# Kernel optimization log

Hardware: AMD Instinct MI355X
Metric: run time of the kernel (lower is better)

The kernel has to match this reference:

```python
import jax, jax.numpy as jnp
import numpy as np

EPS = 1e-9


def setup_inputs() -> dict:
    key = jax.random.key(0)
    k1, k2, k3 = jax.random.split(key, 3)
    B, N, E, F_IN, F_OUT = 8, 2048, 1024, 256, 256
    x = jax.random.normal(k1, (B, N, F_IN), dtype=jnp.float32)
    H = jax.random.uniform(k2, (B, N, E), dtype=jnp.float32)  # soft incidence matrix
    weight = jax.random.normal(k3, (F_IN, F_OUT), dtype=jnp.float32) * (1.0 / np.sqrt(F_OUT))
    return {"x": x, "H": H, "weight": weight}


def reference(x, H, weight):
    # x: [B, N, Fin], H: [B, N, E], weight: [Fin, Fout]
    # Torch builds diag_embed(Dv_inv)/diag_embed(De_inv) and uses dense bmm;
    # mathematically identical to elementwise row-scaling, done here directly.
    Dv = jnp.sum(H, axis=2)                       # [B, N]  (= bmm(H, ones))
    De = jnp.sum(H, axis=1)                       # [B, E]
    Dv_inv = 1.0 / (Dv + EPS)
    De_inv = 1.0 / (De + EPS)
    xw = jnp.matmul(x, weight)                    # [B, N, Fout]
    HTX = jnp.einsum('bne,bnf->bef', H, xw)       # H^T @ X
    HDeHTX = jnp.einsum('bne,bef->bnf', H, De_inv[:, :, None] * HTX)
    out = Dv_inv[:, :, None] * HDeHTX             # [B, N, Fout]
    # dropout in eval mode (identity); relu kept
    return jax.nn.relu(out)
```

## Files before the change

### kernel.cpp

```cpp
#include <hip/hip_runtime.h>
#include <stdint.h>


typedef __bf16 bf16x8 __attribute__((ext_vector_type(8)));
typedef float f32x4 __attribute__((ext_vector_type(4)));

#define PADK 72

__device__ __forceinline__ uint16_t f2b(float f) {
  __bf16 h = (__bf16)f;
  return __builtin_bit_cast(uint16_t, h);
}

__device__ __forceinline__ f32x4 mfma16(bf16x8 a, bf16x8 b, f32x4 c) {
  return __builtin_amdgcn_mfma_f32_16x16x32_bf16(a, b, c, 0, 0, 0);
}

__device__ __forceinline__ void gload16(const void* src, void* dst) {
  __builtin_amdgcn_global_load_lds(
      (const __attribute__((address_space(1))) void*)src,
      (__attribute__((address_space(3))) void*)dst, 16, 0, 0);
}

#define PIPE_WAITN(N) do { \
    asm volatile("s_waitcnt vmcnt(" #N ")" ::: "memory"); \
    __builtin_amdgcn_s_barrier(); \
    __builtin_amdgcn_sched_barrier(0); \
  } while (0)

__global__ __launch_bounds__(256) void k_prep_w(const float* __restrict__ W,
    uint16_t* __restrict__ Wt) {
  __shared__ __align__(16) uint16_t T[64 * 68];
  const int k0 = blockIdx.x * 64, f0 = blockIdx.y * 64;
  const int t = threadIdx.x;
  const int r0 = (t >> 4) * 4, cc = (t & 15) * 4;
  float vv[4][4];
  #pragma unroll
  for (int i = 0; i < 4; ++i) {
    float4 q = *(const float4*)(W + (size_t)(k0 + r0 + i) * 256 + f0 + cc);
    vv[i][0] = q.x; vv[i][1] = q.y; vv[i][2] = q.z; vv[i][3] = q.w;
  }
  #pragma unroll
  for (int j = 0; j < 4; ++j) {
    union { uint16_t s[4]; uint2 u; } p;
    #pragma unroll
    for (int i = 0; i < 4; ++i) p.s[i] = f2b(vv[i][j]);
    *(uint2*)&T[(cc + j) * 68 + r0] = p.u;
  }
  __syncthreads();
  const int er = t >> 2, c2 = (t & 3) * 16;
  union { uint16_t s[16]; uint4 q[2]; } o;
  #pragma unroll
  for (int m = 0; m < 4; ++m)
    *(uint2*)&o.s[m * 4] = *(const uint2*)&T[er * 68 + c2 + m * 4];
  uint16_t* dst = Wt + (size_t)(f0 + er) * 256 + k0 + c2;
  *(uint4*)dst = o.q[0];
  *(uint4*)(dst + 8) = o.q[1];
}

__global__ __launch_bounds__(256) void k_prep_h(const float* __restrict__ H,
    uint16_t* __restrict__ Hbt, uint16_t* __restrict__ Hb,
    float* __restrict__ DvPart, float* __restrict__ DePart) {
  __shared__ __align__(16) uint16_t T[64 * 68];
  __shared__ float cs[4][64];
  const int n0 = blockIdx.x * 64, e0 = blockIdx.y * 64, b = blockIdx.z;
  const int t = threadIdx.x, lane = t & 63, wave = t >> 6;
  const int r0 = (t >> 4) * 4;
  const int cc = (t & 15) * 4;
  float vv[4][4];
  float dv[4];
  float de0 = 0.f, de1 = 0.f, de2 = 0.f, de3 = 0.f;
  #pragma unroll
  for (int i = 0; i < 4; ++i) {
    float4 q = *(const float4*)(H + ((size_t)b * 2048 + n0 + r0 + i) * 1024 + e0 + cc);
    vv[i][0] = q.x; vv[i][1] = q.y; vv[i][2] = q.z; vv[i][3] = q.w;
    float rs = (q.x + q.y) + (q.z + q.w);
    rs += __shfl_xor(rs, 1); rs += __shfl_xor(rs, 2);
    rs += __shfl_xor(rs, 4); rs += __shfl_xor(rs, 8);
    dv[i] = rs;
    de0 += q.x; de1 += q.y; de2 += q.z; de3 += q.w;
  }
  #pragma unroll
  for (int i = 0; i < 4; ++i) {
    union { uint16_t s[4]; uint2 u; } p;
    #pragma unroll
    for (int j = 0; j < 4; ++j) p.s[j] = f2b(vv[i][j]);
    *(uint2*)(Hb + ((size_t)b * 2048 + n0 + r0 + i) * 1024 + e0 + cc) = p.u;
  }
  #pragma unroll
  for (int j = 0; j < 4; ++j) {
    union { uint16_t s[4]; uint2 u; } p;
    #pragma unroll
    for (int i = 0; i < 4; ++i) p.s[i] = f2b(vv[i][j]);
    *(uint2*)&T[(cc + j) * 68 + r0] = p.u;
  }
  de0 += __shfl_xor(de0, 16); de0 += __shfl_xor(de0, 32);
  de1 += __shfl_xor(de1, 16); de1 += __shfl_xor(de1, 32);
  de2 += __shfl_xor(de2, 16); de2 += __shfl_xor(de2, 32);
  de3 += __shfl_xor(de3, 16); de3 += __shfl_xor(de3, 32);
  if (lane < 16) *(float4*)&cs[wave][cc] = make_float4(de0, de1, de2, de3);
  if ((lane & 15) == 0) {
    #pragma unroll
    for (int i = 0; i < 4; ++i)
      DvPart[((size_t)b * 2048 + n0 + r0 + i) * 16 + blockIdx.y] = dv[i];
  }
  __syncthreads();
  const int er = t >> 2, c2 = (t & 3) * 16;
  union { uint16_t s[16]; uint4 q[2]; } o;
  #pragma unroll
  for (int m = 0; m < 4; ++m)
    *(uint2*)&o.s[m * 4] = *(const uint2*)&T[er * 68 + c2 + m * 4];
  uint16_t* dst = Hbt + ((size_t)b * 1024 + e0 + er) * 2048 + n0 + c2;
  *(uint4*)dst = o.q[0];
  *(uint4*)(dst + 8) = o.q[1];
  if (t < 64) {
    float s = (cs[0][t] + cs[1][t]) + (cs[2][t] + cs[3][t]);
    DePart[((size_t)b * 1024 + e0 + t) * 32 + blockIdx.x] = s;
  }
}

__global__ __launch_bounds__(256) void k_gemm1(const float* __restrict__ X,
    const uint16_t* __restrict__ Wt, uint16_t* __restrict__ XWt) {
  __shared__ __align__(16) uint16_t As[2][128 * 64];
  __shared__ __align__(16) uint16_t Bs[2][64 * PADK];
  const int n0 = blockIdx.x * 64, f0 = blockIdx.y * 128, b = blockIdx.z;
  const int t = threadIdx.x, lane = t & 63, wave = t >> 6;
  const int l15 = lane & 15, lq = lane >> 4;
  const int rlane = lane >> 3;
  const int srcswz = ((lane & 7) ^ rlane) << 3;
  const uint16_t* Ag = Wt + (size_t)f0 * 256;
  const int br = t >> 2, kc = (t & 3) * 16;
  const float* Xg = X + ((size_t)b * 2048 + n0 + br) * 256 + kc;
  float4 RX[4];
  auto stageA = [&](uint16_t* Ad, int kt) {
    const int k0 = kt * 64;
    #pragma unroll
    for (int i = 0; i < 4; ++i) {
      const int r = wave * 32 + i * 8;
      gload16(Ag + (size_t)(r + rlane) * 256 + k0 + srcswz, Ad + r * 64);
    }
  };
  auto gloadB = [&](int kt) {
    const float* s = Xg + kt * 64;
    #pragma unroll
    for (int q = 0; q < 4; ++q) RX[q] = *(const float4*)(s + q * 4);
  };
  auto writeB = [&](uint16_t* Bd) {
    uint16_t* d = Bd + br * PADK + kc;
    const float* f = (const float*)RX;
    #pragma unroll
    for (int q = 0; q < 2; ++q) {
      union { uint16_t s[8]; uint4 u; } p;
      #pragma unroll
      for (int j = 0; j < 8; ++j) p.s[j] = f2b(f[q * 8 + j]);
      *(uint4*)(d + q * 8) = p.u;
    }
  };
  f32x4 acc[4][2] = {};
  auto compute = [&](const uint16_t* Ad, const uint16_t* Bd) {
    #pragma unroll
    for (int h = 0; h < 2; ++h) {
      bf16x8 af[4], bf[2];
      #pragma unroll
      for (int i = 0; i < 4; ++i) {
        const int r = (wave >> 1) * 64 + i * 16 + l15;
        af[i] = *(const bf16x8*)(Ad + r * 64 + ((((h << 2) | lq) ^ (r & 7)) << 3));
      }
      #pragma unroll
      for (int j = 0; j < 2; ++j) {
        const int r = (wave & 1) * 32 + j * 16 + l15;
        bf[j] = *(const bf16x8*)(Bd + r * PADK + h * 32 + lq * 8);
      }
      #pragma unroll
      for (int i = 0; i < 4; ++i)
        #pragma unroll
        for (int j = 0; j < 2; ++j)
          acc[i][j] = mfma16(af[i], bf[j], acc[i][j]);
    }
  };
  stageA(As[0], 0); gloadB(0); writeB(Bs[0]);
  __syncthreads();
  for (int kt = 0; kt < 4; kt += 2) {
    stageA(As[1], kt + 1); gloadB(kt + 1);
    compute(As[0], Bs[0]);
    writeB(Bs[1]);
    __syncthreads();
    if (kt + 2 < 4) { stageA(As[0], kt + 2); gloadB(kt + 2); }
    compute(As[1], Bs[1]);
    if (kt + 2 < 4) writeB(Bs[0]);
    __syncthreads();
  }
  #pragma unroll
  for (int i = 0; i < 4; ++i) {
    const int fr = f0 + (wave >> 1) * 64 + i * 16 + lq * 4;
    #pragma unroll
    for (int j = 0; j < 2; ++j) {
      const int col = n0 + (wave & 1) * 32 + j * 16 + l15;
      #pragma unroll
      for (int reg = 0; reg < 4; ++reg)
        XWt[((size_t)b * 256 + fr + reg) * 2048 + col] = f2b(acc[i][j][reg]);
    }
  }
}

__global__ __launch_bounds__(512) void k_gemm2(const uint16_t* __restrict__ Hbt,
    const uint16_t* __restrict__ XWt, const float* __restrict__ DePart,
    uint16_t* __restrict__ Yt) {
  __shared__ __align__(16) uint16_t As[3][256 * 32];
  __shared__ __align__(16) uint16_t Bs[3][64 * 32];
  __shared__ float sde[64];
  const int e0 = blockIdx.x * 64, b = blockIdx.z;
  const int t = threadIdx.x, lane = t & 63, wave = t >> 6;
  const int l15 = lane & 15, lq = lane >> 4;
  const int wf = wave >> 1, we = wave & 1;
  const int ri = lane >> 2, slot = lane & 3;
  const int ksw = (slot ^ ((ri >> 1) & 3)) * 8;
  const uint16_t* Ag = XWt + (size_t)b * 256 * 2048;
  const uint16_t* Bg = Hbt + ((size_t)b * 1024 + e0) * 2048;
  auto stage = [&](uint16_t* Ad, uint16_t* Bd, int kt) {
    const int k0 = kt * 32;
    const int a0 = wave * 2;
    gload16(Ag + (size_t)(a0 * 16 + ri) * 2048 + k0 + ksw, Ad + a0 * 512);
    gload16(Ag + (size_t)(a0 * 16 + 16 + ri) * 2048 + k0 + ksw, Ad + (a0 + 1) * 512);
    const int bb = wave >> 1;
    gload16(Bg + (size_t)(bb * 16 + ri) * 2048 + k0 + ksw, Bd + bb * 512);
  };
  f32x4 acc[4][2] = {};
  auto compute = [&](const uint16_t* Ad, const uint16_t* Bd) {
    bf16x8 af[4], bf[2];
    #pragma unroll
    for (int i = 0; i < 4; ++i) {
      const int r = wf * 64 + i * 16 + l15;
      af[i] = *(const bf16x8*)(Ad + r * 32 + ((lq ^ ((r >> 1) & 3)) * 8));
    }
    #pragma unroll
    for (int j = 0; j < 2; ++j) {
      const int r = we * 32 + j * 16 + l15;
      bf[j] = *(const bf16x8*)(Bd + r * 32 + ((lq ^ ((r >> 1) & 3)) * 8));
    }
    #pragma unroll
    for (int i = 0; i < 4; ++i)
      #pragma unroll
      for (int j = 0; j < 2; ++j)
        acc[i][j] = mfma16(af[i], bf[j], acc[i][j]);
  };
  if (t < 64) {
    const float* p = DePart + ((size_t)b * 1024 + e0 + t) * 32;
    float4 a0 = *(const float4*)(p + 0),  a1 = *(const float4*)(p + 4);
    float4 a2 = *(const float4*)(p + 8),  a3 = *(const float4*)(p + 12);
    float4 a4 = *(const float4*)(p + 16), a5 = *(const float4*)(p + 20);
    float4 a6 = *(const float4*)(p + 24), a7 = *(const float4*)(p + 28);
    float s = (((a0.x + a0.y) + (a0.z + a0.w)) + ((a1.x + a1.y) + (a1.z + a1.w)))
            + (((a2.x + a2.y) + (a2.z + a2.w)) + ((a3.x + a3.y) + (a3.z + a3.w)))
            + ((((a4.x + a4.y) + (a4.z + a4.w)) + ((a5.x + a5.y) + (a5.z + a5.w)))
            + (((a6.x + a6.y) + (a6.z + a6.w)) + ((a7.x + a7.y) + (a7.z + a7.w))));
    sde[t] = 1.f / (s + 1e-9f);
  }
  stage(As[0], Bs[0], 0);
  stage(As[1], Bs[1], 1);
  __syncthreads();
  const int NT = 64;
  uint16_t *cA = As[0], *nA = As[1], *fA = As[2];
  uint16_t *cB = Bs[0], *nB = Bs[1], *fB = Bs[2];
  for (int kt = 0; kt < NT - 2; ++kt) {
    stage(fA, fB, kt + 2);
    compute(cA, cB);
    PIPE_WAITN(3);
    uint16_t* t1 = cA; cA = nA; nA = fA; fA = t1;
    uint16_t* t2 = cB; cB = nB; nB = fB; fB = t2;
  }
  compute(cA, cB);
  PIPE_WAITN(0);
  compute(nA, nB);
  #pragma unroll
  for (int i = 0; i < 4; ++i) {
    const int fr = wf * 64 + i * 16 + lq * 4;
    #pragma unroll
    for (int j = 0; j < 2; ++j) {
      const int el = we * 32 + j * 16 + l15;
      const float sc = sde[el];
      uint16_t* dst = Yt + ((size_t)b * 256 + fr) * 1024 + e0 + el;
      #pragma unroll
      for (int reg = 0; reg < 4; ++reg)
        dst[(size_t)reg * 1024] = f2b(acc[i][j][reg] * sc);
    }
  }
}

__global__ __launch_bounds__(256) void k_gemm3(const uint16_t* __restrict__ Hb,
    const uint16_t* __restrict__ Yt, const float* __restrict__ DvPart,
    float* __restrict__ out) {
  __shared__ __align__(16) uint16_t As[3][128 * 32];
  __shared__ __align__(16) uint16_t Bs[3][128 * 32];
  __shared__ float sdv[128];
  const int n0 = blockIdx.x * 128, f0 = blockIdx.y * 128, b = blockIdx.z;
  const int t = threadIdx.x, lane = t & 63, wave = t >> 6;
  const int l15 = lane & 15, lq = lane >> 4;
  const int wn = wave >> 1, wf = wave & 1;
  const int ri = lane >> 2, slot = lane & 3;
  const int ksw = (slot ^ ((ri >> 1) & 3)) * 8;
  const uint16_t* Ag = Hb + ((size_t)b * 2048 + n0) * 1024;
  const uint16_t* Bg = Yt + ((size_t)b * 256 + f0) * 1024;
  auto stage = [&](uint16_t* Ad, uint16_t* Bd, int kt) {
    const int k0 = kt * 32;
    const int c0 = wave * 2;
    #pragma unroll
    for (int i = 0; i < 2; ++i) {
      gload16(Ag + (size_t)((c0 + i) * 16 + ri) * 1024 + k0 + ksw, Ad + (c0 + i) * 512);
      gload16(Bg + (size_t)((c0 + i) * 16 + ri) * 1024 + k0 + ksw, Bd + (c0 + i) * 512);
    }
  };
  f32x4 acc[4][4] = {};
  auto compute = [&](const uint16_t* Ad, const uint16_t* Bd) {
    bf16x8 af[4], bf[4];
    #pragma unroll
    for (int i = 0; i < 4; ++i) {
      const int r = wn * 64 + i * 16 + l15;
      af[i] = *(const bf16x8*)(Ad + r * 32 + ((lq ^ ((r >> 1) & 3)) * 8));
    }
    #pragma unroll
    for (int j = 0; j < 4; ++j) {
      const int r = wf * 64 + j * 16 + l15;
      bf[j] = *(const bf16x8*)(Bd + r * 32 + ((lq ^ ((r >> 1) & 3)) * 8));
    }
    #pragma unroll
    for (int i = 0; i < 4; ++i)
      #pragma unroll
      for (int j = 0; j < 4; ++j)
        acc[i][j] = mfma16(af[i], bf[j], acc[i][j]);
  };
  if (t < 128) {
    const float* p = DvPart + ((size_t)b * 2048 + n0 + t) * 16;
    float4 a0 = *(const float4*)(p + 0),  a1 = *(const float4*)(p + 4);
    float4 a2 = *(const float4*)(p + 8),  a3 = *(const float4*)(p + 12);
    float s = (((a0.x + a0.y) + (a0.z + a0.w)) + ((a1.x + a1.y) + (a1.z + a1.w)))
            + (((a2.x + a2.y) + (a2.z + a2.w)) + ((a3.x + a3.y) + (a3.z + a3.w)));
    sdv[t] = 1.f / (s + 1e-9f);
  }
  stage(As[0], Bs[0], 0);
  stage(As[1], Bs[1], 1);
  __syncthreads();
  const int NT = 32;
  uint16_t *cA = As[0], *nA = As[1], *fA = As[2];
  uint16_t *cB = Bs[0], *nB = Bs[1], *fB = Bs[2];
  for (int kt = 0; kt < NT - 2; ++kt) {
    stage(fA, fB, kt + 2);
    compute(cA, cB);
    PIPE_WAITN(4);
    uint16_t* t1 = cA; cA = nA; nA = fA; fA = t1;
    uint16_t* t2 = cB; cB = nB; nB = fB; fB = t2;
  }
  compute(cA, cB);
  PIPE_WAITN(0);
  compute(nA, nB);
  #pragma unroll
  for (int i = 0; i < 4; ++i) {
    const int nl = wn * 64 + i * 16 + lq * 4;
    #pragma unroll
    for (int reg = 0; reg < 4; ++reg) {
      const int row = n0 + nl + reg;
      const float sc = sdv[nl + reg];
      #pragma unroll
      for (int j = 0; j < 4; ++j) {
        const int col = f0 + wf * 64 + j * 16 + l15;
        const float v = acc[i][j][reg] * sc;
        out[((size_t)b * 2048 + row) * 256 + col] = v > 0.f ? v : 0.f;
      }
    }
  }
}

extern "C" void kernel_launch(void* const* d_in, const int* in_sizes, int n_in,
                              void* d_out, int out_size, void* d_ws, size_t ws_size,
                              hipStream_t stream) {
  (void)in_sizes; (void)n_in; (void)out_size;
  const float* x = (const float*)d_in[0];
  const float* H = (const float*)d_in[1];
  const float* W = (const float*)d_in[2];
  float* out = (float*)d_out;

  if (ws_size < 81920000) return;
  char* ws = (char*)d_ws;
  uint16_t* Hbt    = (uint16_t*)(ws);
  uint16_t* Hb     = (uint16_t*)(ws + 33554432);
  uint16_t* XWt    = (uint16_t*)(ws + 67108864);
  uint16_t* Yt     = (uint16_t*)(ws + 75497472);
  float*    DvPart = (float*)(ws + 79691776);
  float*    DePart = (float*)(ws + 80740352);
  uint16_t* Wt     = (uint16_t*)(ws + 81788928);

  k_prep_w<<<dim3(4, 4),      256, 0, stream>>>(W, Wt);
  k_prep_h<<<dim3(32, 16, 8), 256, 0, stream>>>(H, Hbt, Hb, DvPart, DePart);
  k_gemm1 <<<dim3(32, 2, 8),  256, 0, stream>>>(x, Wt, XWt);
  k_gemm2 <<<dim3(16, 1, 8),  512, 0, stream>>>(Hbt, XWt, DePart, Yt);
  k_gemm3 <<<dim3(16, 2, 8),  256, 0, stream>>>(Hb, Yt, DvPart, out);
}
```

Before: 92.38 us.

## Retile gemm2 into 64x128 tiles with K=64 steps and more blocks

The H^T·XW GEMM now uses 256-thread blocks, each computing a 64(F)×128(E) output tile, in place of 512-thread blocks that covered all 256 features for 64 edges. The K step doubles to 64, with an 8-way XOR swizzle in LDS and a deeper wait count. The grid grows from 128 to 256 blocks to fill more CUs and halve the barriers per K. In exchange, each block re-reads H tiles across 4 F-blocks, which raises global and L2 traffic for H.

```diff
diff --git a/kernel.cpp b/kernel.cpp
--- a/kernel.cpp
+++ b/kernel.cpp
@@ -203,48 +203,56 @@
   }
 }
 
-__global__ __launch_bounds__(512) void k_gemm2(const uint16_t* __restrict__ Hbt,
+__global__ __launch_bounds__(256) void k_gemm2(const uint16_t* __restrict__ Hbt,
     const uint16_t* __restrict__ XWt, const float* __restrict__ DePart,
     uint16_t* __restrict__ Yt) {
-  __shared__ __align__(16) uint16_t As[3][256 * 32];
-  __shared__ __align__(16) uint16_t Bs[3][64 * 32];
-  __shared__ float sde[64];
-  const int e0 = blockIdx.x * 64, b = blockIdx.z;
+  __shared__ __align__(16) uint16_t As[3][64 * 64];
+  __shared__ __align__(16) uint16_t Bs[3][128 * 64];
+  __shared__ float sde[128];
+  const int e0 = blockIdx.x * 128, f0 = blockIdx.y * 64, b = blockIdx.z;
   const int t = threadIdx.x, lane = t & 63, wave = t >> 6;
   const int l15 = lane & 15, lq = lane >> 4;
   const int wf = wave >> 1, we = wave & 1;
-  const int ri = lane >> 2, slot = lane & 3;
-  const int ksw = (slot ^ ((ri >> 1) & 3)) * 8;
-  const uint16_t* Ag = XWt + (size_t)b * 256 * 2048;
+  const int ri8 = lane >> 3, sl8 = lane & 7;
+  const int ksw = (sl8 ^ ri8) << 3;
+  const uint16_t* Ag = XWt + ((size_t)b * 256 + f0) * 2048;
   const uint16_t* Bg = Hbt + ((size_t)b * 1024 + e0) * 2048;
   auto stage = [&](uint16_t* Ad, uint16_t* Bd, int kt) {
-    const int k0 = kt * 32;
-    const int a0 = wave * 2;
-    gload16(Ag + (size_t)(a0 * 16 + ri) * 2048 + k0 + ksw, Ad + a0 * 512);
-    gload16(Ag + (size_t)(a0 * 16 + 16 + ri) * 2048 + k0 + ksw, Ad + (a0 + 1) * 512);
-    const int bb = wave >> 1;
-    gload16(Bg + (size_t)(bb * 16 + ri) * 2048 + k0 + ksw, Bd + bb * 512);
-  };
-  f32x4 acc[4][2] = {};
+    const int k0 = kt * 64;
+    #pragma unroll
+    for (int i = 0; i < 2; ++i) {
+      const int c = wave * 2 + i;
+      gload16(Ag + (size_t)(c * 8 + ri8) * 2048 + k0 + ksw, Ad + c * 512);
+    }
+    #pragma unroll
+    for (int i = 0; i < 4; ++i) {
+      const int c = wave * 4 + i;
+      gload16(Bg + (size_t)(c * 8 + ri8) * 2048 + k0 + ksw, Bd + c * 512);
+    }
+  };
+  f32x4 acc[2][4] = {};
   auto compute = [&](const uint16_t* Ad, const uint16_t* Bd) {
-    bf16x8 af[4], bf[2];
-    #pragma unroll
-    for (int i = 0; i < 4; ++i) {
-      const int r = wf * 64 + i * 16 + l15;
-      af[i] = *(const bf16x8*)(Ad + r * 32 + ((lq ^ ((r >> 1) & 3)) * 8));
-    }
-    #pragma unroll
-    for (int j = 0; j < 2; ++j) {
-      const int r = we * 32 + j * 16 + l15;
-      bf[j] = *(const bf16x8*)(Bd + r * 32 + ((lq ^ ((r >> 1) & 3)) * 8));
-    }
-    #pragma unroll
-    for (int i = 0; i < 4; ++i)
-      #pragma unroll
-      for (int j = 0; j < 2; ++j)
-        acc[i][j] = mfma16(af[i], bf[j], acc[i][j]);
-  };
-  if (t < 64) {
+    #pragma unroll
+    for (int h = 0; h < 2; ++h) {
+      bf16x8 af[2], bf[4];
+      #pragma unroll
+      for (int i = 0; i < 2; ++i) {
+        const int r = wf * 32 + i * 16 + l15;
+        af[i] = *(const bf16x8*)(Ad + r * 64 + ((((h << 2) | lq) ^ (r & 7)) << 3));
+      }
+      #pragma unroll
+      for (int j = 0; j < 4; ++j) {
+        const int r = we * 64 + j * 16 + l15;
+        bf[j] = *(const bf16x8*)(Bd + r * 64 + ((((h << 2) | lq) ^ (r & 7)) << 3));
+      }
+      #pragma unroll
+      for (int i = 0; i < 2; ++i)
+        #pragma unroll
+        for (int j = 0; j < 4; ++j)
+          acc[i][j] = mfma16(af[i], bf[j], acc[i][j]);
+    }
+  };
+  if (t < 128) {
     const float* p = DePart + ((size_t)b * 1024 + e0 + t) * 32;
     float4 a0 = *(const float4*)(p + 0),  a1 = *(const float4*)(p + 4);
     float4 a2 = *(const float4*)(p + 8),  a3 = *(const float4*)(p + 12);
@@ -259,13 +267,13 @@
   stage(As[0], Bs[0], 0);
   stage(As[1], Bs[1], 1);
   __syncthreads();
-  const int NT = 64;
+  const int NT = 32;
   uint16_t *cA = As[0], *nA = As[1], *fA = As[2];
   uint16_t *cB = Bs[0], *nB = Bs[1], *fB = Bs[2];
   for (int kt = 0; kt < NT - 2; ++kt) {
     stage(fA, fB, kt + 2);
     compute(cA, cB);
-    PIPE_WAITN(3);
+    PIPE_WAITN(6);
     uint16_t* t1 = cA; cA = nA; nA = fA; fA = t1;
     uint16_t* t2 = cB; cB = nB; nB = fB; fB = t2;
   }
@@ -273,11 +281,11 @@
   PIPE_WAITN(0);
   compute(nA, nB);
   #pragma unroll
-  for (int i = 0; i < 4; ++i) {
-    const int fr = wf * 64 + i * 16 + lq * 4;
-    #pragma unroll
-    for (int j = 0; j < 2; ++j) {
-      const int el = we * 32 + j * 16 + l15;
+  for (int i = 0; i < 2; ++i) {
+    const int fr = f0 + wf * 32 + i * 16 + lq * 4;
+    #pragma unroll
+    for (int j = 0; j < 4; ++j) {
+      const int el = we * 64 + j * 16 + l15;
       const float sc = sde[el];
       uint16_t* dst = Yt + ((size_t)b * 256 + fr) * 1024 + e0 + el;
       #pragma unroll
@@ -392,6 +400,6 @@
   k_prep_w<<<dim3(4, 4),      256, 0, stream>>>(W, Wt);
   k_prep_h<<<dim3(32, 16, 8), 256, 0, stream>>>(H, Hbt, Hb, DvPart, DePart);
   k_gemm1 <<<dim3(32, 2, 8),  256, 0, stream>>>(x, Wt, XWt);
-  k_gemm2 <<<dim3(16, 1, 8),  512, 0, stream>>>(Hbt, XWt, DePart, Yt);
+  k_gemm2 <<<dim3(8, 4, 8),   256, 0, stream>>>(Hbt, XWt, DePart, Yt);
   k_gemm3 <<<dim3(16, 2, 8),  256, 0, stream>>>(Hb, Yt, DvPart, out);
 }
```

Result: faster. 80.85 us (-12.5%).
